# Optimization experiments

Hardware: AMD Instinct MI355X
Metric: run time of the kernel (lower is better)

Reference implementation:

```python
import jax, jax.numpy as jnp
import numpy as np
from jax import lax

EPS = 1e-5

def _zpool(x):
    # cat(max over channel, mean over channel) -> [B,2,H,W]
    return jnp.concatenate([x.max(axis=1, keepdims=True), x.mean(axis=1, keepdims=True)], axis=1)

def _gate(x, w, g, b, m, v):
    # ZPool -> 7x7 conv (2->1, same pad) -> inference BN -> sigmoid -> scale input
    z = _zpool(x)
    y = lax.conv_general_dilated(z, w, (1, 1), [(3, 3), (3, 3)],
                                 dimension_numbers=('NCHW', 'OIHW', 'NCHW'))
    scale = g / jnp.sqrt(v + EPS)
    y = (y - m[None, :, None, None]) * scale[None, :, None, None] + b[None, :, None, None]
    return x * jax.nn.sigmoid(y)


def setup_inputs() -> dict:
    key = jax.random.key(0)
    ks = jax.random.split(key, 8)
    B, C, H, W = 8, 256, 64, 64
    inp = {
        'x': jax.random.normal(ks[0], (B, C, H, W), dtype=jnp.float32),
        'w_cw': jax.random.normal(ks[1], (1, 2, 7, 7), dtype=jnp.float32) * 0.1,
        'g_cw': jnp.ones((1,), jnp.float32), 'b_cw': jnp.zeros((1,), jnp.float32),
        'm_cw': jnp.zeros((1,), jnp.float32), 'v_cw': jnp.ones((1,), jnp.float32),
        'w_hc': jax.random.normal(ks[2], (1, 2, 7, 7), dtype=jnp.float32) * 0.1,
        'g_hc': jnp.ones((1,), jnp.float32), 'b_hc': jnp.zeros((1,), jnp.float32),
        'm_hc': jnp.zeros((1,), jnp.float32), 'v_hc': jnp.ones((1,), jnp.float32),
        'w_hw': jax.random.normal(ks[3], (1, 2, 7, 7), dtype=jnp.float32) * 0.1,
        'g_hw': jnp.ones((1,), jnp.float32), 'b_hw': jnp.zeros((1,), jnp.float32),
        'm_hw': jnp.zeros((1,), jnp.float32), 'v_hw': jnp.ones((1,), jnp.float32),
        'w1d': jax.random.normal(ks[4], (3, 1, 7), dtype=jnp.float32) * 0.1,
    }
    return inp


def reference(x, w_cw, g_cw, b_cw, m_cw, v_cw,
              w_hc, g_hc, b_hc, m_hc, v_hc,
              w_hw, g_hw, b_hw, m_hw, v_hw, w1d):
    # branch 1: attend over (C) with H as channel dim
    b1 = _gate(x.transpose(0, 2, 1, 3), w_cw, g_cw, b_cw, m_cw, v_cw).transpose(0, 2, 1, 3)
    # branch 2: attend with W as channel dim
    b2 = _gate(x.transpose(0, 3, 2, 1), w_hc, g_hc, b_hc, m_hc, v_hc).transpose(0, 3, 2, 1)
    # branch 3: spatial attention in native layout
    b3 = _gate(x, w_hw, g_hw, b_hw, m_hw, v_hw)

    x_out = (b1 + b2 + b3) / 3.0
    pooled = x_out.mean(axis=(2, 3))                     # [B, C]
    logits = lax.conv_general_dilated(pooled[:, None, :], w1d, (1,), [(3, 3)],
                                      dimension_numbers=('NCH', 'OIH', 'NCH'))  # [B,3,C]
    wts = jax.nn.softmax(logits, axis=1)[..., None, None]  # [B,3,C,1,1]
    branches = jnp.stack([b1, b2, b3], axis=1)             # [B,3,C,H,W]
    return (wts * branches).sum(axis=1)
```

## Files before the change

### kernel.cpp

```cpp
#include <hip/hip_runtime.h>
#include <math.h>

#define BB 8
#define CC 256
#define HH 64
#define WW 64
#define EPS 1e-5f

__global__ __launch_bounds__(256) void pool_kernel(
    const float* __restrict__ x,
    float* __restrict__ z1max, float* __restrict__ z1mean,
    float* __restrict__ z2max, float* __restrict__ z2mean,
    float* __restrict__ z3max, float* __restrict__ z3mean)
{
    __shared__ float smem[HH * 65 + 512];
    int blk = blockIdx.x;
    int t = threadIdx.x;

    if (blk < BB * CC) {
        int bc = blk;
        int b = bc >> 8, c = bc & 255;
        const float4* xt4 = (const float4*)x + (size_t)bc * 1024;
        float* tile = smem;
        float* red  = smem + HH * 65;

        #pragma unroll
        for (int i = 0; i < 4; ++i) {
            int idx = t + i * 256;
            float4 v = xt4[idx];
            int h = idx >> 4, w0 = (idx & 15) * 4;
            float* d = &tile[h * 65 + w0];
            d[0] = v.x; d[1] = v.y; d[2] = v.z; d[3] = v.w;
        }
        __syncthreads();

        {
            int w = t & 63, hg = t >> 6;
            float m = -INFINITY, s = 0.f;
            #pragma unroll
            for (int i = 0; i < 16; ++i) {
                float v = tile[(hg * 16 + i) * 65 + w];
                m = fmaxf(m, v); s += v;
            }
            red[t] = m; red[256 + t] = s;
        }
        __syncthreads();
        if (t < 64) {
            int w = t;
            float m = red[w], s = red[256 + w];
            #pragma unroll
            for (int g = 1; g < 4; ++g) { m = fmaxf(m, red[g * 64 + w]); s += red[256 + g * 64 + w]; }
            z1max [bc * WW + w] = m;
            z1mean[bc * WW + w] = s * (1.f / 64.f);
        }
        __syncthreads();

        {
            int h = t & 63, wg = t >> 6;
            float m = -INFINITY, s = 0.f;
            #pragma unroll
            for (int i = 0; i < 16; ++i) {
                float v = tile[h * 65 + wg * 16 + i];
                m = fmaxf(m, v); s += v;
            }
            red[t] = m; red[256 + t] = s;
        }
        __syncthreads();
        if (t < 64) {
            int h = t;
            float m = red[h], s = red[256 + h];
            #pragma unroll
            for (int g = 1; g < 4; ++g) { m = fmaxf(m, red[g * 64 + h]); s += red[256 + g * 64 + h]; }
            z2max [(b * HH + h) * CC + c] = m;
            z2mean[(b * HH + h) * CC + c] = s * (1.f / 64.f);
        }
    } else {
        int bh = blk - BB * CC;
        int b = bh >> 6, h = bh & 63;
        int wq = t & 15, cg = t >> 4;

        const float4* base = (const float4*)x
            + ((size_t)b * CC * HH * WW + (size_t)h * WW) / 4 + wq;
        float4 m = make_float4(-INFINITY, -INFINITY, -INFINITY, -INFINITY);
        float4 s = make_float4(0.f, 0.f, 0.f, 0.f);
        #pragma unroll 4
        for (int i = 0; i < 16; ++i) {
            float4 v = base[(size_t)(cg * 16 + i) * 1024];
            m.x = fmaxf(m.x, v.x); m.y = fmaxf(m.y, v.y);
            m.z = fmaxf(m.z, v.z); m.w = fmaxf(m.w, v.w);
            s.x += v.x; s.y += v.y; s.z += v.z; s.w += v.w;
        }
        float4* mred = (float4*)smem;
        float4* sred = (float4*)smem + 256;
        mred[t] = m; sred[t] = s;
        __syncthreads();
        if (t < 16) {
            float4 mm = mred[t], ss = sred[t];
            #pragma unroll
            for (int g = 1; g < 16; ++g) {
                float4 mv = mred[g * 16 + t], sv = sred[g * 16 + t];
                mm.x = fmaxf(mm.x, mv.x); mm.y = fmaxf(mm.y, mv.y);
                mm.z = fmaxf(mm.z, mv.z); mm.w = fmaxf(mm.w, mv.w);
                ss.x += sv.x; ss.y += sv.y; ss.z += sv.z; ss.w += sv.w;
            }
            ss.x *= (1.f / 256.f); ss.y *= (1.f / 256.f);
            ss.z *= (1.f / 256.f); ss.w *= (1.f / 256.f);
            *(float4*)(z3max  + bh * WW + t * 4) = mm;
            *(float4*)(z3mean + bh * WW + t * 4) = ss;
        }
    }
}

__global__ __launch_bounds__(256) void conv_gate_kernel(
    const float* __restrict__ z1max, const float* __restrict__ z1mean,
    const float* __restrict__ w0p, const float* g0, const float* b0,
    const float* m0, const float* v0, float* __restrict__ s1,
    const float* __restrict__ z2max, const float* __restrict__ z2mean,
    const float* __restrict__ w1p, const float* g1, const float* b1,
    const float* m1, const float* v1, float* __restrict__ s2,
    const float* __restrict__ z3max, const float* __restrict__ z3mean,
    const float* __restrict__ w2p, const float* g2, const float* b2,
    const float* m2, const float* v2, float* __restrict__ s3)
{
    int br = blockIdx.y;
    const float *zm, *za, *wp, *gp, *bp, *mp, *vp;
    float* sp; int R, Cw;
    if (br == 0)      { zm=z1max; za=z1mean; wp=w0p; gp=g0; bp=b0; mp=m0; vp=v0; sp=s1; R=CC; Cw=WW; }
    else if (br == 1) { zm=z2max; za=z2mean; wp=w1p; gp=g1; bp=b1; mp=m1; vp=v1; sp=s2; R=HH; Cw=CC; }
    else              { zm=z3max; za=z3mean; wp=w2p; gp=g2; bp=b2; mp=m2; vp=v2; sp=s3; R=HH; Cw=WW; }

    int total = BB * R * Cw;
    int o = blockIdx.x * 256 + threadIdx.x;
    if (o >= total) return;

    int b   = o / (R * Cw);
    int rem = o - b * R * Cw;
    int r   = rem / Cw;
    int col = rem - r * Cw;

    const float* zmb = zm + (size_t)b * R * Cw;
    const float* zab = za + (size_t)b * R * Cw;

    float acc = 0.f;
    #pragma unroll
    for (int dr = 0; dr < 7; ++dr) {
        int rr = r + dr - 3;
        if (rr < 0 || rr >= R) continue;
        #pragma unroll
        for (int dc = 0; dc < 7; ++dc) {
            int cc = col + dc - 3;
            if (cc < 0 || cc >= Cw) continue;
            float wm = wp[dr * 7 + dc];
            float wa = wp[49 + dr * 7 + dc];
            acc += wm * zmb[rr * Cw + cc] + wa * zab[rr * Cw + cc];
        }
    }
    float scale = gp[0] * rsqrtf(vp[0] + EPS);
    float y = (acc - mp[0]) * scale + bp[0];
    sp[o] = 1.f / (1.f + __expf(-y));
}

__global__ __launch_bounds__(256) void pooled_kernel(
    const float* __restrict__ x,
    const float* __restrict__ s1, const float* __restrict__ z1mean,
    const float* __restrict__ s2, const float* __restrict__ z2mean,
    const float* __restrict__ s3, float* __restrict__ pooled)
{
    int bc = blockIdx.x;
    int b = bc >> 8, c = bc & 255;
    int t = threadIdx.x;

    const float4* xt4 = (const float4*)x  + (size_t)bc * 1024;
    const float4* s34 = (const float4*)s3 + (size_t)b * 1024;

    float acc = 0.f;
    #pragma unroll
    for (int i = 0; i < 4; ++i) {
        float4 xv = xt4[t + i * 256];
        float4 sv = s34[t + i * 256];
        acc += xv.x * sv.x + xv.y * sv.y + xv.z * sv.z + xv.w * sv.w;
    }
    if (t < 64) {
        int w = t;
        acc += 64.f * s1[bc * WW + w] * z1mean[bc * WW + w];
    } else if (t < 128) {
        int h = t - 64;
        int idx = (b * HH + h) * CC + c;
        acc += 64.f * s2[idx] * z2mean[idx];
    }
    #pragma unroll
    for (int off = 32; off >= 1; off >>= 1) acc += __shfl_down(acc, off);
    __shared__ float r[4];
    if ((t & 63) == 0) r[t >> 6] = acc;
    __syncthreads();
    if (t == 0) pooled[bc] = (r[0] + r[1] + r[2] + r[3]) * (1.f / (4096.f * 3.f));
}

__global__ __launch_bounds__(256) void final_kernel(
    const float* __restrict__ x,
    const float* __restrict__ s1, const float* __restrict__ s2,
    const float* __restrict__ s3, const float* __restrict__ pooled,
    const float* __restrict__ w1d, float* __restrict__ out)
{
    int i4 = blockIdx.x * 256 + threadIdx.x;
    int w0   = (i4 & 15) * 4;
    int rest = i4 >> 4;
    int h = rest & 63; rest >>= 6;
    int c = rest & 255;
    int b = rest >> 8;

    float lg0 = 0.f, lg1 = 0.f, lg2 = 0.f;
    #pragma unroll
    for (int j = 0; j < 7; ++j) {
        int cc = c + j - 3;
        float p = (cc >= 0 && cc < CC) ? pooled[b * CC + cc] : 0.f;
        lg0 += w1d[j] * p;
        lg1 += w1d[7 + j] * p;
        lg2 += w1d[14 + j] * p;
    }
    float mx = fmaxf(lg0, fmaxf(lg1, lg2));
    float e0 = __expf(lg0 - mx), e1 = __expf(lg1 - mx), e2 = __expf(lg2 - mx);
    float inv = 1.f / (e0 + e1 + e2);
    float k0 = e0 * inv, k1 = e1 * inv, k2 = e2 * inv;

    const float4 x4  = *(const float4*)(x  + (size_t)i4 * 4);
    const float4 s1v = *(const float4*)(s1 + ((size_t)(b * CC + c)) * WW + w0);
    const float  s2v = s2[(b * HH + h) * CC + c];
    const float4 s3v = *(const float4*)(s3 + ((size_t)(b * HH + h)) * WW + w0);

    float4 o;
    o.x = x4.x * (k0 * s1v.x + k1 * s2v + k2 * s3v.x);
    o.y = x4.y * (k0 * s1v.y + k1 * s2v + k2 * s3v.y);
    o.z = x4.z * (k0 * s1v.z + k1 * s2v + k2 * s3v.z);
    o.w = x4.w * (k0 * s1v.w + k1 * s2v + k2 * s3v.w);
    *(float4*)(out + (size_t)i4 * 4) = o;
}

extern "C" void kernel_launch(void* const* d_in, const int* in_sizes, int n_in,
                              void* d_out, int out_size, void* d_ws, size_t ws_size,
                              hipStream_t stream)
{
    const float* x    = (const float*)d_in[0];
    const float* w_cw = (const float*)d_in[1];
    const float* g_cw = (const float*)d_in[2];
    const float* b_cw = (const float*)d_in[3];
    const float* m_cw = (const float*)d_in[4];
    const float* v_cw = (const float*)d_in[5];
    const float* w_hc = (const float*)d_in[6];
    const float* g_hc = (const float*)d_in[7];
    const float* b_hc = (const float*)d_in[8];
    const float* m_hc = (const float*)d_in[9];
    const float* v_hc = (const float*)d_in[10];
    const float* w_hw = (const float*)d_in[11];
    const float* g_hw = (const float*)d_in[12];
    const float* b_hw = (const float*)d_in[13];
    const float* m_hw = (const float*)d_in[14];
    const float* v_hw = (const float*)d_in[15];
    const float* w1d  = (const float*)d_in[16];
    float* out = (float*)d_out;

    float* ws = (float*)d_ws;
    const size_t N1 = (size_t)BB * CC * WW;
    const size_t N2 = (size_t)BB * HH * CC;
    const size_t N3 = (size_t)BB * HH * WW;
    float* z1max  = ws;
    float* z1mean = z1max  + N1;
    float* z2max  = z1mean + N1;
    float* z2mean = z2max  + N2;
    float* z3max  = z2mean + N2;
    float* z3mean = z3max  + N3;
    float* s1     = z3mean + N3;
    float* s2     = s1 + N1;
    float* s3     = s2 + N2;
    float* pooled = s3 + N3;

    pool_kernel<<<BB * CC + BB * HH, 256, 0, stream>>>(
        x, z1max, z1mean, z2max, z2mean, z3max, z3mean);

    conv_gate_kernel<<<dim3((BB * CC * WW + 255) / 256, 3), 256, 0, stream>>>(
        z1max, z1mean, w_cw, g_cw, b_cw, m_cw, v_cw, s1,
        z2max, z2mean, w_hc, g_hc, b_hc, m_hc, v_hc, s2,
        z3max, z3mean, w_hw, g_hw, b_hw, m_hw, v_hw, s3);

    pooled_kernel<<<BB * CC, 256, 0, stream>>>(
        x, s1, z1mean, s2, z2mean, s3, pooled);

    final_kernel<<<(BB * CC * HH * WW / 4) / 256, 256, 0, stream>>>(
        x, s1, s2, s3, pooled, w1d, out);
}
```

Baseline: 150.5 us.

## Fuse four kernels into one persistent cooperative kernel with grid syncs

Replaces the four separate launches (pool, conv-gate, pooled, final) with one cooperative kernel of 512 blocks that loops over work items and separates the stages with grid.sync(). This removes per-launch overhead and the gaps between kernels. In exchange, parallelism is capped at a fixed grid, each stage is processed in grid-stride loops, and the grid-wide barriers have their own cost. The cooperative launch can fail if the 512 blocks cannot all be resident at once.

```diff
diff --git a/kernel.cpp b/kernel.cpp
--- a/kernel.cpp
+++ b/kernel.cpp
@@ -1,29 +1,75 @@
 #include <hip/hip_runtime.h>
+#include <hip/hip_cooperative_groups.h>
 #include <math.h>
+
+namespace cg = cooperative_groups;
 
 #define BB 8
 #define CC 256
 #define HH 64
 #define WW 64
 #define EPS 1e-5f
-
-__global__ __launch_bounds__(256) void pool_kernel(
-    const float* __restrict__ x,
-    float* __restrict__ z1max, float* __restrict__ z1mean,
-    float* __restrict__ z2max, float* __restrict__ z2mean,
-    float* __restrict__ z3max, float* __restrict__ z3mean)
+#define GRID 512
+#define NTHR 256
+
+struct Params {
+    const float *x;
+    const float *w_cw, *g_cw, *b_cw, *m_cw, *v_cw;
+    const float *w_hc, *g_hc, *b_hc, *m_hc, *v_hc;
+    const float *w_hw, *g_hw, *b_hw, *m_hw, *v_hw;
+    const float *w1d;
+    float *z1max, *z1mean, *z2max, *z2mean, *z3max, *z3mean;
+    float *s1, *s2, *s3, *pooled, *out;
+};
+
+__device__ __forceinline__ void conv_one(
+    const float* __restrict__ zm, const float* __restrict__ za,
+    const float* __restrict__ wp, const float* gp, const float* bp,
+    const float* mp, const float* vp, float* __restrict__ sp,
+    int R, int Cw, int o)
+{
+    int b   = o / (R * Cw);
+    int rem = o - b * R * Cw;
+    int r   = rem / Cw;
+    int col = rem - r * Cw;
+    const float* zmb = zm + (size_t)b * R * Cw;
+    const float* zab = za + (size_t)b * R * Cw;
+    float acc = 0.f;
+    #pragma unroll
+    for (int dr = 0; dr < 7; ++dr) {
+        int rr = r + dr - 3;
+        if (rr < 0 || rr >= R) continue;
+        #pragma unroll
+        for (int dc = 0; dc < 7; ++dc) {
+            int cc2 = col + dc - 3;
+            if (cc2 < 0 || cc2 >= Cw) continue;
+            acc += wp[dr * 7 + dc]      * zmb[rr * Cw + cc2]
+                 + wp[49 + dr * 7 + dc] * zab[rr * Cw + cc2];
+        }
+    }
+    float scale = gp[0] * rsqrtf(vp[0] + EPS);
+    float y = (acc - mp[0]) * scale + bp[0];
+    sp[o] = 1.f / (1.f + __expf(-y));
+}
+
+__global__ __launch_bounds__(256, 2) void fused_kernel(Params p)
 {
     __shared__ float smem[HH * 65 + 512];
+    __shared__ float r4[4];
+    cg::grid_group grid = cg::this_grid();
+    int t   = threadIdx.x;
     int blk = blockIdx.x;
-    int t = threadIdx.x;
-
-    if (blk < BB * CC) {
-        int bc = blk;
+    int tid = blk * NTHR + t;
+
+    float* tile = smem;
+    float* red  = smem + HH * 65;
+
+    #pragma unroll 1
+    for (int pidx = 0; pidx < 4; ++pidx) {
+        int bc = blk + pidx * GRID;
         int b = bc >> 8, c = bc & 255;
-        const float4* xt4 = (const float4*)x + (size_t)bc * 1024;
-        float* tile = smem;
-        float* red  = smem + HH * 65;
-
+        const float4* xt4 = (const float4*)p.x + (size_t)bc * 1024;
+        __syncthreads();
         #pragma unroll
         for (int i = 0; i < 4; ++i) {
             int idx = t + i * 256;
@@ -33,7 +79,6 @@
             d[0] = v.x; d[1] = v.y; d[2] = v.z; d[3] = v.w;
         }
         __syncthreads();
-
         {
             int w = t & 63, hg = t >> 6;
             float m = -INFINITY, s = 0.f;
@@ -46,15 +91,13 @@
         }
         __syncthreads();
         if (t < 64) {
-            int w = t;
-            float m = red[w], s = red[256 + w];
-            #pragma unroll
-            for (int g = 1; g < 4; ++g) { m = fmaxf(m, red[g * 64 + w]); s += red[256 + g * 64 + w]; }
-            z1max [bc * WW + w] = m;
-            z1mean[bc * WW + w] = s * (1.f / 64.f);
-        }
-        __syncthreads();
-
+            float m = red[t], s = red[256 + t];
+            #pragma unroll
+            for (int g = 1; g < 4; ++g) { m = fmaxf(m, red[g * 64 + t]); s += red[256 + g * 64 + t]; }
+            p.z1max [bc * WW + t] = m;
+            p.z1mean[bc * WW + t] = s * (1.f / 64.f);
+        }
+        __syncthreads();
         {
             int h = t & 63, wg = t >> 6;
             float m = -INFINITY, s = 0.f;
@@ -67,25 +110,26 @@
         }
         __syncthreads();
         if (t < 64) {
-            int h = t;
-            float m = red[h], s = red[256 + h];
-            #pragma unroll
-            for (int g = 1; g < 4; ++g) { m = fmaxf(m, red[g * 64 + h]); s += red[256 + g * 64 + h]; }
-            z2max [(b * HH + h) * CC + c] = m;
-            z2mean[(b * HH + h) * CC + c] = s * (1.f / 64.f);
-        }
-    } else {
-        int bh = blk - BB * CC;
+            float m = red[t], s = red[256 + t];
+            #pragma unroll
+            for (int g = 1; g < 4; ++g) { m = fmaxf(m, red[g * 64 + t]); s += red[256 + g * 64 + t]; }
+            p.z2max [(b * HH + t) * CC + c] = m;
+            p.z2mean[(b * HH + t) * CC + c] = s * (1.f / 64.f);
+        }
+    }
+
+    {
+        __syncthreads();
+        int bh = blk;
         int b = bh >> 6, h = bh & 63;
-        int wq = t & 15, cg = t >> 4;
-
-        const float4* base = (const float4*)x
+        int wq = t & 15, cgp = t >> 4;
+        const float4* base = (const float4*)p.x
             + ((size_t)b * CC * HH * WW + (size_t)h * WW) / 4 + wq;
         float4 m = make_float4(-INFINITY, -INFINITY, -INFINITY, -INFINITY);
         float4 s = make_float4(0.f, 0.f, 0.f, 0.f);
         #pragma unroll 4
         for (int i = 0; i < 16; ++i) {
-            float4 v = base[(size_t)(cg * 16 + i) * 1024];
+            float4 v = base[(size_t)(cgp * 16 + i) * 1024];
             m.x = fmaxf(m.x, v.x); m.y = fmaxf(m.y, v.y);
             m.z = fmaxf(m.z, v.z); m.w = fmaxf(m.w, v.w);
             s.x += v.x; s.y += v.y; s.z += v.z; s.w += v.w;
@@ -105,186 +149,131 @@
             }
             ss.x *= (1.f / 256.f); ss.y *= (1.f / 256.f);
             ss.z *= (1.f / 256.f); ss.w *= (1.f / 256.f);
-            *(float4*)(z3max  + bh * WW + t * 4) = mm;
-            *(float4*)(z3mean + bh * WW + t * 4) = ss;
-        }
-    }
-}
-
-__global__ __launch_bounds__(256) void conv_gate_kernel(
-    const float* __restrict__ z1max, const float* __restrict__ z1mean,
-    const float* __restrict__ w0p, const float* g0, const float* b0,
-    const float* m0, const float* v0, float* __restrict__ s1,
-    const float* __restrict__ z2max, const float* __restrict__ z2mean,
-    const float* __restrict__ w1p, const float* g1, const float* b1,
-    const float* m1, const float* v1, float* __restrict__ s2,
-    const float* __restrict__ z3max, const float* __restrict__ z3mean,
-    const float* __restrict__ w2p, const float* g2, const float* b2,
-    const float* m2, const float* v2, float* __restrict__ s3)
-{
-    int br = blockIdx.y;
-    const float *zm, *za, *wp, *gp, *bp, *mp, *vp;
-    float* sp; int R, Cw;
-    if (br == 0)      { zm=z1max; za=z1mean; wp=w0p; gp=g0; bp=b0; mp=m0; vp=v0; sp=s1; R=CC; Cw=WW; }
-    else if (br == 1) { zm=z2max; za=z2mean; wp=w1p; gp=g1; bp=b1; mp=m1; vp=v1; sp=s2; R=HH; Cw=CC; }
-    else              { zm=z3max; za=z3mean; wp=w2p; gp=g2; bp=b2; mp=m2; vp=v2; sp=s3; R=HH; Cw=WW; }
-
-    int total = BB * R * Cw;
-    int o = blockIdx.x * 256 + threadIdx.x;
-    if (o >= total) return;
-
-    int b   = o / (R * Cw);
-    int rem = o - b * R * Cw;
-    int r   = rem / Cw;
-    int col = rem - r * Cw;
-
-    const float* zmb = zm + (size_t)b * R * Cw;
-    const float* zab = za + (size_t)b * R * Cw;
-
-    float acc = 0.f;
-    #pragma unroll
-    for (int dr = 0; dr < 7; ++dr) {
-        int rr = r + dr - 3;
-        if (rr < 0 || rr >= R) continue;
-        #pragma unroll
-        for (int dc = 0; dc < 7; ++dc) {
-            int cc = col + dc - 3;
-            if (cc < 0 || cc >= Cw) continue;
-            float wm = wp[dr * 7 + dc];
-            float wa = wp[49 + dr * 7 + dc];
-            acc += wm * zmb[rr * Cw + cc] + wa * zab[rr * Cw + cc];
-        }
-    }
-    float scale = gp[0] * rsqrtf(vp[0] + EPS);
-    float y = (acc - mp[0]) * scale + bp[0];
-    sp[o] = 1.f / (1.f + __expf(-y));
-}
-
-__global__ __launch_bounds__(256) void pooled_kernel(
-    const float* __restrict__ x,
-    const float* __restrict__ s1, const float* __restrict__ z1mean,
-    const float* __restrict__ s2, const float* __restrict__ z2mean,
-    const float* __restrict__ s3, float* __restrict__ pooled)
-{
-    int bc = blockIdx.x;
-    int b = bc >> 8, c = bc & 255;
-    int t = threadIdx.x;
-
-    const float4* xt4 = (const float4*)x  + (size_t)bc * 1024;
-    const float4* s34 = (const float4*)s3 + (size_t)b * 1024;
-
-    float acc = 0.f;
-    #pragma unroll
-    for (int i = 0; i < 4; ++i) {
-        float4 xv = xt4[t + i * 256];
-        float4 sv = s34[t + i * 256];
-        acc += xv.x * sv.x + xv.y * sv.y + xv.z * sv.z + xv.w * sv.w;
-    }
-    if (t < 64) {
-        int w = t;
-        acc += 64.f * s1[bc * WW + w] * z1mean[bc * WW + w];
-    } else if (t < 128) {
-        int h = t - 64;
-        int idx = (b * HH + h) * CC + c;
-        acc += 64.f * s2[idx] * z2mean[idx];
-    }
-    #pragma unroll
-    for (int off = 32; off >= 1; off >>= 1) acc += __shfl_down(acc, off);
-    __shared__ float r[4];
-    if ((t & 63) == 0) r[t >> 6] = acc;
-    __syncthreads();
-    if (t == 0) pooled[bc] = (r[0] + r[1] + r[2] + r[3]) * (1.f / (4096.f * 3.f));
-}
-
-__global__ __launch_bounds__(256) void final_kernel(
-    const float* __restrict__ x,
-    const float* __restrict__ s1, const float* __restrict__ s2,
-    const float* __restrict__ s3, const float* __restrict__ pooled,
-    const float* __restrict__ w1d, float* __restrict__ out)
-{
-    int i4 = blockIdx.x * 256 + threadIdx.x;
-    int w0   = (i4 & 15) * 4;
-    int rest = i4 >> 4;
-    int h = rest & 63; rest >>= 6;
-    int c = rest & 255;
-    int b = rest >> 8;
-
-    float lg0 = 0.f, lg1 = 0.f, lg2 = 0.f;
-    #pragma unroll
-    for (int j = 0; j < 7; ++j) {
-        int cc = c + j - 3;
-        float p = (cc >= 0 && cc < CC) ? pooled[b * CC + cc] : 0.f;
-        lg0 += w1d[j] * p;
-        lg1 += w1d[7 + j] * p;
-        lg2 += w1d[14 + j] * p;
-    }
-    float mx = fmaxf(lg0, fmaxf(lg1, lg2));
-    float e0 = __expf(lg0 - mx), e1 = __expf(lg1 - mx), e2 = __expf(lg2 - mx);
-    float inv = 1.f / (e0 + e1 + e2);
-    float k0 = e0 * inv, k1 = e1 * inv, k2 = e2 * inv;
-
-    const float4 x4  = *(const float4*)(x  + (size_t)i4 * 4);
-    const float4 s1v = *(const float4*)(s1 + ((size_t)(b * CC + c)) * WW + w0);
-    const float  s2v = s2[(b * HH + h) * CC + c];
-    const float4 s3v = *(const float4*)(s3 + ((size_t)(b * HH + h)) * WW + w0);
-
-    float4 o;
-    o.x = x4.x * (k0 * s1v.x + k1 * s2v + k2 * s3v.x);
-    o.y = x4.y * (k0 * s1v.y + k1 * s2v + k2 * s3v.y);
-    o.z = x4.z * (k0 * s1v.z + k1 * s2v + k2 * s3v.z);
-    o.w = x4.w * (k0 * s1v.w + k1 * s2v + k2 * s3v.w);
-    *(float4*)(out + (size_t)i4 * 4) = o;
+            *(float4*)(p.z3max  + bh * WW + t * 4) = mm;
+            *(float4*)(p.z3mean + bh * WW + t * 4) = ss;
+        }
+    }
+
+    grid.sync();
+
+    #pragma unroll 1
+    for (int o = tid; o < 294912; o += GRID * NTHR) {
+        if (o < 131072)
+            conv_one(p.z1max, p.z1mean, p.w_cw, p.g_cw, p.b_cw, p.m_cw, p.v_cw, p.s1, CC, WW, o);
+        else if (o < 262144)
+            conv_one(p.z2max, p.z2mean, p.w_hc, p.g_hc, p.b_hc, p.m_hc, p.v_hc, p.s2, HH, CC, o - 131072);
+        else
+            conv_one(p.z3max, p.z3mean, p.w_hw, p.g_hw, p.b_hw, p.m_hw, p.v_hw, p.s3, HH, WW, o - 262144);
+    }
+
+    grid.sync();
+
+    #pragma unroll 1
+    for (int pidx = 0; pidx < 4; ++pidx) {
+        int bc = blk + pidx * GRID;
+        int b = bc >> 8, c = bc & 255;
+        const float4* xt4 = (const float4*)p.x  + (size_t)bc * 1024;
+        const float4* s34 = (const float4*)p.s3 + (size_t)b * 1024;
+        float acc = 0.f;
+        #pragma unroll
+        for (int i = 0; i < 4; ++i) {
+            float4 xv = xt4[t + i * 256];
+            float4 sv = s34[t + i * 256];
+            acc += xv.x * sv.x + xv.y * sv.y + xv.z * sv.z + xv.w * sv.w;
+        }
+        if (t < 64) {
+            acc += 64.f * p.s1[bc * WW + t] * p.z1mean[bc * WW + t];
+        } else if (t < 128) {
+            int idx = (b * HH + (t - 64)) * CC + c;
+            acc += 64.f * p.s2[idx] * p.z2mean[idx];
+        }
+        #pragma unroll
+        for (int off = 32; off >= 1; off >>= 1) acc += __shfl_down(acc, off);
+        if ((t & 63) == 0) r4[t >> 6] = acc;
+        __syncthreads();
+        if (t == 0) p.pooled[bc] = (r4[0] + r4[1] + r4[2] + r4[3]) * (1.f / (4096.f * 3.f));
+        __syncthreads();
+    }
+
+    grid.sync();
+
+    #pragma unroll 1
+    for (int j = 0; j < 16; ++j) {
+        int i4 = j * (GRID * NTHR) + tid;
+        int w0   = (i4 & 15) * 4;
+        int rest = i4 >> 4;
+        int h = rest & 63; rest >>= 6;
+        int c = rest & 255;
+        int b = rest >> 8;
+
+        float lg0 = 0.f, lg1 = 0.f, lg2 = 0.f;
+        #pragma unroll
+        for (int jj = 0; jj < 7; ++jj) {
+            int cc2 = c + jj - 3;
+            float pv = (cc2 >= 0 && cc2 < CC) ? p.pooled[b * CC + cc2] : 0.f;
+            lg0 += p.w1d[jj] * pv;
+            lg1 += p.w1d[7 + jj] * pv;
+            lg2 += p.w1d[14 + jj] * pv;
+        }
+        float mx = fmaxf(lg0, fmaxf(lg1, lg2));
+        float e0 = __expf(lg0 - mx), e1 = __expf(lg1 - mx), e2 = __expf(lg2 - mx);
+        float inv = 1.f / (e0 + e1 + e2);
+        float k0 = e0 * inv, k1 = e1 * inv, k2 = e2 * inv;
+
+        const float4 x4  = *(const float4*)(p.x  + (size_t)i4 * 4);
+        const float4 s1v = *(const float4*)(p.s1 + ((size_t)(b * CC + c)) * WW + w0);
+        const float  s2v = p.s2[(b * HH + h) * CC + c];
+        const float4 s3v = *(const float4*)(p.s3 + ((size_t)(b * HH + h)) * WW + w0);
+
+        float4 o;
+        o.x = x4.x * (k0 * s1v.x + k1 * s2v + k2 * s3v.x);
+        o.y = x4.y * (k0 * s1v.y + k1 * s2v + k2 * s3v.y);
+        o.z = x4.z * (k0 * s1v.z + k1 * s2v + k2 * s3v.z);
+        o.w = x4.w * (k0 * s1v.w + k1 * s2v + k2 * s3v.w);
+        *(float4*)(p.out + (size_t)i4 * 4) = o;
+    }
 }
 
 extern "C" void kernel_launch(void* const* d_in, const int* in_sizes, int n_in,
                               void* d_out, int out_size, void* d_ws, size_t ws_size,
                               hipStream_t stream)
 {
-    const float* x    = (const float*)d_in[0];
-    const float* w_cw = (const float*)d_in[1];
-    const float* g_cw = (const float*)d_in[2];
-    const float* b_cw = (const float*)d_in[3];
-    const float* m_cw = (const float*)d_in[4];
-    const float* v_cw = (const float*)d_in[5];
-    const float* w_hc = (const float*)d_in[6];
-    const float* g_hc = (const float*)d_in[7];
-    const float* b_hc = (const float*)d_in[8];
-    const float* m_hc = (const float*)d_in[9];
-    const float* v_hc = (const float*)d_in[10];
-    const float* w_hw = (const float*)d_in[11];
-    const float* g_hw = (const float*)d_in[12];
-    const float* b_hw = (const float*)d_in[13];
-    const float* m_hw = (const float*)d_in[14];
-    const float* v_hw = (const float*)d_in[15];
-    const float* w1d  = (const float*)d_in[16];
-    float* out = (float*)d_out;
+    Params pp;
+    pp.x    = (const float*)d_in[0];
+    pp.w_cw = (const float*)d_in[1];
+    pp.g_cw = (const float*)d_in[2];
+    pp.b_cw = (const float*)d_in[3];
+    pp.m_cw = (const float*)d_in[4];
+    pp.v_cw = (const float*)d_in[5];
+    pp.w_hc = (const float*)d_in[6];
+    pp.g_hc = (const float*)d_in[7];
+    pp.b_hc = (const float*)d_in[8];
+    pp.m_hc = (const float*)d_in[9];
+    pp.v_hc = (const float*)d_in[10];
+    pp.w_hw = (const float*)d_in[11];
+    pp.g_hw = (const float*)d_in[12];
+    pp.b_hw = (const float*)d_in[13];
+    pp.m_hw = (const float*)d_in[14];
+    pp.v_hw = (const float*)d_in[15];
+    pp.w1d  = (const float*)d_in[16];
+    pp.out  = (float*)d_out;
 
     float* ws = (float*)d_ws;
     const size_t N1 = (size_t)BB * CC * WW;
     const size_t N2 = (size_t)BB * HH * CC;
     const size_t N3 = (size_t)BB * HH * WW;
-    float* z1max  = ws;
-    float* z1mean = z1max  + N1;
-    float* z2max  = z1mean + N1;
-    float* z2mean = z2max  + N2;
-    float* z3max  = z2mean + N2;
-    float* z3mean = z3max  + N3;
-    float* s1     = z3mean + N3;
-    float* s2     = s1 + N1;
-    float* s3     = s2 + N2;
-    float* pooled = s3 + N3;
-
-    pool_kernel<<<BB * CC + BB * HH, 256, 0, stream>>>(
-        x, z1max, z1mean, z2max, z2mean, z3max, z3mean);
-
-    conv_gate_kernel<<<dim3((BB * CC * WW + 255) / 256, 3), 256, 0, stream>>>(
-        z1max, z1mean, w_cw, g_cw, b_cw, m_cw, v_cw, s1,
-        z2max, z2mean, w_hc, g_hc, b_hc, m_hc, v_hc, s2,
-        z3max, z3mean, w_hw, g_hw, b_hw, m_hw, v_hw, s3);
-
-    pooled_kernel<<<BB * CC, 256, 0, stream>>>(
-        x, s1, z1mean, s2, z2mean, s3, pooled);
-
-    final_kernel<<<(BB * CC * HH * WW / 4) / 256, 256, 0, stream>>>(
-        x, s1, s2, s3, pooled, w1d, out);
+    pp.z1max  = ws;
+    pp.z1mean = pp.z1max  + N1;
+    pp.z2max  = pp.z1mean + N1;
+    pp.z2mean = pp.z2max  + N2;
+    pp.z3max  = pp.z2mean + N2;
+    pp.z3mean = pp.z3max  + N3;
+    pp.s1     = pp.z3mean + N3;
+    pp.s2     = pp.s1 + N1;
+    pp.s3     = pp.s2 + N2;
+    pp.pooled = pp.s3 + N3;
+
+    void* args[] = { &pp };
+    hipLaunchCooperativeKernel((const void*)fused_kernel, dim3(GRID), dim3(NTHR),
+                               args, 0, stream);
 }
```

New measurement: 363.4 us. 141% more time.

## Fuse pooled reduction into gate kernel via atomic accumulation

Applied to the files above, without the earlier changes.

Merges the conv-gate and pooled-mean kernels into one launch. Each branch adds its contribution to the pooled vector with atomics, and the branch-3 blocks compute the x·s3 dot product per (b,h) row. The pooled buffer is zeroed inside the pool kernel, and the 1/12288 normalisation moves into the final kernel. This removes one launch and the pooled kernel's separate pass over x, at the cost of many atomic adds (branch 2 adds one per element) and a non-deterministic summation order.

```diff
diff --git a/kernel.cpp b/kernel.cpp
--- a/kernel.cpp
+++ b/kernel.cpp
@@ -6,16 +6,20 @@
 #define HH 64
 #define WW 64
 #define EPS 1e-5f
+#define PSCALE (1.f / 12288.f)
 
 __global__ __launch_bounds__(256) void pool_kernel(
     const float* __restrict__ x,
     float* __restrict__ z1max, float* __restrict__ z1mean,
     float* __restrict__ z2max, float* __restrict__ z2mean,
-    float* __restrict__ z3max, float* __restrict__ z3mean)
+    float* __restrict__ z3max, float* __restrict__ z3mean,
+    float* __restrict__ pooled)
 {
     __shared__ float smem[HH * 65 + 512];
     int blk = blockIdx.x;
     int t = threadIdx.x;
+
+    if (blk < 8) pooled[blk * 256 + t] = 0.f;
 
     if (blk < BB * CC) {
         int bc = blk;
@@ -46,12 +50,11 @@
         }
         __syncthreads();
         if (t < 64) {
-            int w = t;
-            float m = red[w], s = red[256 + w];
-            #pragma unroll
-            for (int g = 1; g < 4; ++g) { m = fmaxf(m, red[g * 64 + w]); s += red[256 + g * 64 + w]; }
-            z1max [bc * WW + w] = m;
-            z1mean[bc * WW + w] = s * (1.f / 64.f);
+            float m = red[t], s = red[256 + t];
+            #pragma unroll
+            for (int g = 1; g < 4; ++g) { m = fmaxf(m, red[g * 64 + t]); s += red[256 + g * 64 + t]; }
+            z1max [bc * WW + t] = m;
+            z1mean[bc * WW + t] = s * (1.f / 64.f);
         }
         __syncthreads();
 
@@ -67,17 +70,16 @@
         }
         __syncthreads();
         if (t < 64) {
-            int h = t;
-            float m = red[h], s = red[256 + h];
-            #pragma unroll
-            for (int g = 1; g < 4; ++g) { m = fmaxf(m, red[g * 64 + h]); s += red[256 + g * 64 + h]; }
-            z2max [(b * HH + h) * CC + c] = m;
-            z2mean[(b * HH + h) * CC + c] = s * (1.f / 64.f);
+            float m = red[t], s = red[256 + t];
+            #pragma unroll
+            for (int g = 1; g < 4; ++g) { m = fmaxf(m, red[g * 64 + t]); s += red[256 + g * 64 + t]; }
+            z2max [(b * HH + t) * CC + c] = m;
+            z2mean[(b * HH + t) * CC + c] = s * (1.f / 64.f);
         }
     } else {
         int bh = blk - BB * CC;
         int b = bh >> 6, h = bh & 63;
-        int wq = t & 15, cg = t >> 4;
+        int wq = t & 15, cgp = t >> 4;
 
         const float4* base = (const float4*)x
             + ((size_t)b * CC * HH * WW + (size_t)h * WW) / 4 + wq;
@@ -85,7 +87,7 @@
         float4 s = make_float4(0.f, 0.f, 0.f, 0.f);
         #pragma unroll 4
         for (int i = 0; i < 16; ++i) {
-            float4 v = base[(size_t)(cg * 16 + i) * 1024];
+            float4 v = base[(size_t)(cgp * 16 + i) * 1024];
             m.x = fmaxf(m.x, v.x); m.y = fmaxf(m.y, v.y);
             m.z = fmaxf(m.z, v.z); m.w = fmaxf(m.w, v.w);
             s.x += v.x; s.y += v.y; s.z += v.z; s.w += v.w;
@@ -111,7 +113,34 @@
     }
 }
 
-__global__ __launch_bounds__(256) void conv_gate_kernel(
+__device__ __forceinline__ float conv_gate(
+    const float* __restrict__ zm, const float* __restrict__ za,
+    const float* __restrict__ wp, const float* gp, const float* bp,
+    const float* mp, const float* vp,
+    int R, int Cw, int b, int r, int col)
+{
+    const float* zmb = zm + (size_t)b * R * Cw;
+    const float* zab = za + (size_t)b * R * Cw;
+    float acc = 0.f;
+    #pragma unroll
+    for (int dr = 0; dr < 7; ++dr) {
+        int rr = r + dr - 3;
+        if (rr < 0 || rr >= R) continue;
+        #pragma unroll
+        for (int dc = 0; dc < 7; ++dc) {
+            int cc2 = col + dc - 3;
+            if (cc2 < 0 || cc2 >= Cw) continue;
+            acc += wp[dr * 7 + dc]      * zmb[rr * Cw + cc2]
+                 + wp[49 + dr * 7 + dc] * zab[rr * Cw + cc2];
+        }
+    }
+    float scale = gp[0] * rsqrtf(vp[0] + EPS);
+    float y = (acc - mp[0]) * scale + bp[0];
+    return 1.f / (1.f + __expf(-y));
+}
+
+__global__ __launch_bounds__(256) void gate_kernel(
+    const float* __restrict__ x,
     const float* __restrict__ z1max, const float* __restrict__ z1mean,
     const float* __restrict__ w0p, const float* g0, const float* b0,
     const float* m0, const float* v0, float* __restrict__ s1,
@@ -120,80 +149,61 @@
     const float* m1, const float* v1, float* __restrict__ s2,
     const float* __restrict__ z3max, const float* __restrict__ z3mean,
     const float* __restrict__ w2p, const float* g2, const float* b2,
-    const float* m2, const float* v2, float* __restrict__ s3)
-{
-    int br = blockIdx.y;
-    const float *zm, *za, *wp, *gp, *bp, *mp, *vp;
-    float* sp; int R, Cw;
-    if (br == 0)      { zm=z1max; za=z1mean; wp=w0p; gp=g0; bp=b0; mp=m0; vp=v0; sp=s1; R=CC; Cw=WW; }
-    else if (br == 1) { zm=z2max; za=z2mean; wp=w1p; gp=g1; bp=b1; mp=m1; vp=v1; sp=s2; R=HH; Cw=CC; }
-    else              { zm=z3max; za=z3mean; wp=w2p; gp=g2; bp=b2; mp=m2; vp=v2; sp=s3; R=HH; Cw=WW; }
-
-    int total = BB * R * Cw;
-    int o = blockIdx.x * 256 + threadIdx.x;
-    if (o >= total) return;
-
-    int b   = o / (R * Cw);
-    int rem = o - b * R * Cw;
-    int r   = rem / Cw;
-    int col = rem - r * Cw;
-
-    const float* zmb = zm + (size_t)b * R * Cw;
-    const float* zab = za + (size_t)b * R * Cw;
-
-    float acc = 0.f;
-    #pragma unroll
-    for (int dr = 0; dr < 7; ++dr) {
-        int rr = r + dr - 3;
-        if (rr < 0 || rr >= R) continue;
+    const float* m2, const float* v2, float* __restrict__ s3,
+    float* __restrict__ pooled)
+{
+    int blk = blockIdx.x;
+    int t = threadIdx.x;
+
+    if (blk < 512) {
+        int o = blk * 256 + t;
+        int b = o >> 14, rem = o & 16383;
+        int r = rem >> 6, col = o & 63;
+        float v = conv_gate(z1max, z1mean, w0p, g0, b0, m0, v0, CC, WW, b, r, col);
+        s1[o] = v;
+        float prod = v * z1mean[o];
         #pragma unroll
-        for (int dc = 0; dc < 7; ++dc) {
-            int cc = col + dc - 3;
-            if (cc < 0 || cc >= Cw) continue;
-            float wm = wp[dr * 7 + dc];
-            float wa = wp[49 + dr * 7 + dc];
-            acc += wm * zmb[rr * Cw + cc] + wa * zab[rr * Cw + cc];
+        for (int off = 32; off >= 1; off >>= 1) prod += __shfl_down(prod, off);
+        if ((t & 63) == 0) atomicAdd(&pooled[o >> 6], 64.f * prod);
+    } else if (blk < 1024) {
+        int o = (blk - 512) * 256 + t;
+        int b = o >> 14, rem = o & 16383;
+        int r = rem >> 8, col = o & 255;
+        float v = conv_gate(z2max, z2mean, w1p, g1, b1, m1, v1, HH, CC, b, r, col);
+        s2[o] = v;
+        atomicAdd(&pooled[(b << 8) | col], 64.f * v * z2mean[o]);
+    } else {
+        __shared__ float s3row[WW];
+        int bh = blk - 1024;
+        int b = bh >> 6, h = bh & 63;
+        if (t < 64) {
+            float v = conv_gate(z3max, z3mean, w2p, g2, b2, m2, v2, HH, WW, b, h, t);
+            s3[bh * WW + t] = v;
+            s3row[t] = v;
+        }
+        __syncthreads();
+
+        int wv = t >> 6, l = t & 63;
+        int c_local = l >> 2, wsub = l & 3;
+        const float4* s3q4 = (const float4*)s3row;
+
+        #pragma unroll 1
+        for (int pass = 0; pass < 4; ++pass) {
+            int c = pass * 64 + (wv << 4) + c_local;
+            const float4* xr4 = (const float4*)x
+                + ((size_t)(b * 256 + c) * 4096 + h * 64) / 4 + wsub * 4;
+            float acc = 0.f;
+            #pragma unroll
+            for (int j = 0; j < 4; ++j) {
+                float4 xv = xr4[j];
+                float4 sv = s3q4[wsub * 4 + j];
+                acc += xv.x * sv.x + xv.y * sv.y + xv.z * sv.z + xv.w * sv.w;
+            }
+            acc += __shfl_xor(acc, 1);
+            acc += __shfl_xor(acc, 2);
+            if (wsub == 0) atomicAdd(&pooled[b * 256 + c], acc);
         }
     }
-    float scale = gp[0] * rsqrtf(vp[0] + EPS);
-    float y = (acc - mp[0]) * scale + bp[0];
-    sp[o] = 1.f / (1.f + __expf(-y));
-}
-
-__global__ __launch_bounds__(256) void pooled_kernel(
-    const float* __restrict__ x,
-    const float* __restrict__ s1, const float* __restrict__ z1mean,
-    const float* __restrict__ s2, const float* __restrict__ z2mean,
-    const float* __restrict__ s3, float* __restrict__ pooled)
-{
-    int bc = blockIdx.x;
-    int b = bc >> 8, c = bc & 255;
-    int t = threadIdx.x;
-
-    const float4* xt4 = (const float4*)x  + (size_t)bc * 1024;
-    const float4* s34 = (const float4*)s3 + (size_t)b * 1024;
-
-    float acc = 0.f;
-    #pragma unroll
-    for (int i = 0; i < 4; ++i) {
-        float4 xv = xt4[t + i * 256];
-        float4 sv = s34[t + i * 256];
-        acc += xv.x * sv.x + xv.y * sv.y + xv.z * sv.z + xv.w * sv.w;
-    }
-    if (t < 64) {
-        int w = t;
-        acc += 64.f * s1[bc * WW + w] * z1mean[bc * WW + w];
-    } else if (t < 128) {
-        int h = t - 64;
-        int idx = (b * HH + h) * CC + c;
-        acc += 64.f * s2[idx] * z2mean[idx];
-    }
-    #pragma unroll
-    for (int off = 32; off >= 1; off >>= 1) acc += __shfl_down(acc, off);
-    __shared__ float r[4];
-    if ((t & 63) == 0) r[t >> 6] = acc;
-    __syncthreads();
-    if (t == 0) pooled[bc] = (r[0] + r[1] + r[2] + r[3]) * (1.f / (4096.f * 3.f));
 }
 
 __global__ __launch_bounds__(256) void final_kernel(
@@ -211,13 +221,14 @@
 
     float lg0 = 0.f, lg1 = 0.f, lg2 = 0.f;
     #pragma unroll
-    for (int j = 0; j < 7; ++j) {
-        int cc = c + j - 3;
-        float p = (cc >= 0 && cc < CC) ? pooled[b * CC + cc] : 0.f;
-        lg0 += w1d[j] * p;
-        lg1 += w1d[7 + j] * p;
-        lg2 += w1d[14 + j] * p;
+    for (int jj = 0; jj < 7; ++jj) {
+        int cc2 = c + jj - 3;
+        float pv = (cc2 >= 0 && cc2 < CC) ? pooled[b * CC + cc2] : 0.f;
+        lg0 += w1d[jj] * pv;
+        lg1 += w1d[7 + jj] * pv;
+        lg2 += w1d[14 + jj] * pv;
     }
+    lg0 *= PSCALE; lg1 *= PSCALE; lg2 *= PSCALE;
     float mx = fmaxf(lg0, fmaxf(lg1, lg2));
     float e0 = __expf(lg0 - mx), e1 = __expf(lg1 - mx), e2 = __expf(lg2 - mx);
     float inv = 1.f / (e0 + e1 + e2);
@@ -275,15 +286,14 @@
     float* pooled = s3 + N3;
 
     pool_kernel<<<BB * CC + BB * HH, 256, 0, stream>>>(
-        x, z1max, z1mean, z2max, z2mean, z3max, z3mean);
-
-    conv_gate_kernel<<<dim3((BB * CC * WW + 255) / 256, 3), 256, 0, stream>>>(
+        x, z1max, z1mean, z2max, z2mean, z3max, z3mean, pooled);
+
+    gate_kernel<<<1536, 256, 0, stream>>>(
+        x,
         z1max, z1mean, w_cw, g_cw, b_cw, m_cw, v_cw, s1,
         z2max, z2mean, w_hc, g_hc, b_hc, m_hc, v_hc, s2,
-        z3max, z3mean, w_hw, g_hw, b_hw, m_hw, v_hw, s3);
-
-    pooled_kernel<<<BB * CC, 256, 0, stream>>>(
-        x, s1, z1mean, s2, z2mean, s3, pooled);
+        z3max, z3mean, w_hw, g_hw, b_hw, m_hw, v_hw, s3,
+        pooled);
 
     final_kernel<<<(BB * CC * HH * WW / 4) / 256, 256, 0, stream>>>(
         x, s1, s2, s3, pooled, w1d, out);
```

Result: faster. 147.2 us (-2.2%).
